# Kernel optimization log

Hardware: AMD Instinct MI355X
Metric: run time of the kernel (lower is better)

The kernel has to match this reference:

```python
import jax, jax.numpy as jnp
import numpy as np

NEG_SLOPE = 0.2  # PyG GATConv default negative_slope
EPS = 1e-16


def gat_conv(x, edge_index, W, att_src, att_dst, bias, heads, out_c, concat):
    """Faithful PyG GATConv forward (add_self_loops=True).
    x: [N, F_in], edge_index: [2, E] (row 0 = src, row 1 = dst),
    W: [heads*out_c, F_in], att_src/att_dst: [1, heads, out_c], bias: [out]
    """
    N = x.shape[0]
    loop = jnp.arange(N, dtype=edge_index.dtype)
    src = jnp.concatenate([edge_index[0], loop])
    dst = jnp.concatenate([edge_index[1], loop])

    h = (x @ W.T).reshape(N, heads, out_c)            # [N, H, C]
    a_src = jnp.sum(h * att_src, axis=-1)             # [N, H]
    a_dst = jnp.sum(h * att_dst, axis=-1)             # [N, H]

    e = jax.nn.leaky_relu(a_src[src] + a_dst[dst], NEG_SLOPE)   # [E+N, H]
    # numerically-stable segment softmax over incoming edges of dst
    m = jax.ops.segment_max(e, dst, num_segments=N)             # [N, H]
    p = jnp.exp(e - m[dst])
    denom = jax.ops.segment_sum(p, dst, num_segments=N)         # [N, H]
    alpha = p / (denom[dst] + EPS)                              # [E+N, H]

    out = jax.ops.segment_sum(h[src] * alpha[:, :, None], dst, num_segments=N)  # [N, H, C]
    out = out.reshape(N, heads * out_c) if concat else out.mean(axis=1)
    return out + bias


def setup_inputs() -> dict:
    key = jax.random.key(0)
    ks = jax.random.split(key, 11)
    N, E = 100_000, 1_600_000
    in_dim, hid, heads = 128, 64, 2
    s = 0.1
    x = jax.random.normal(ks[0], (N, in_dim), jnp.float32)
    edge_index_l2 = jax.random.randint(ks[1], (2, E), 0, N, dtype=jnp.int32)
    edge_index_l1 = jax.random.randint(ks[2], (2, E), 0, N, dtype=jnp.int32)
    # layer gat_l2: in_dim -> hid per head, heads=2, concat=True
    W2 = jax.random.normal(ks[3], (heads * hid, in_dim), jnp.float32) * s
    att_src2 = jax.random.normal(ks[4], (1, heads, hid), jnp.float32) * s
    att_dst2 = jax.random.normal(ks[5], (1, heads, hid), jnp.float32) * s
    b2 = jnp.zeros((heads * hid,), jnp.float32)
    # layer gat_l1: hid*heads -> hid, 1 head, concat=False
    W1 = jax.random.normal(ks[6], (hid, heads * hid), jnp.float32) * s
    att_src1 = jax.random.normal(ks[7], (1, 1, hid), jnp.float32) * s
    att_dst1 = jax.random.normal(ks[8], (1, 1, hid), jnp.float32) * s
    b1 = jnp.zeros((hid,), jnp.float32)
    return {
        "x": x,
        "edge_index_l1": edge_index_l1,
        "edge_index_l2": edge_index_l2,
        "W2": W2, "att_src2": att_src2, "att_dst2": att_dst2, "b2": b2,
        "W1": W1, "att_src1": att_src1, "att_dst1": att_dst1, "b1": b1,
    }


def reference(x, edge_index_l1, edge_index_l2, W2, att_src2, att_dst2, b2,
              W1, att_src1, att_dst1, b1):
    h = jax.nn.elu(gat_conv(x, edge_index_l2, W2, att_src2, att_dst2, b2,
                            heads=2, out_c=64, concat=True))    # [N, 128]
    h = jax.nn.elu(gat_conv(h, edge_index_l1, W1, att_src1, att_dst1, b1,
                            heads=1, out_c=64, concat=False))   # [N, 64]
    return h
```

## Files before the change

### kernel.cpp

```cpp
#include <hip/hip_runtime.h>
#include <hip/hip_bf16.h>
#include <math.h>

#define LRELU_SLOPE 0.2f
#define EPS 1e-16f
#define BUCK_SHIFT 8
#define BUCK_NODES 256
#define MAXBUCK 512

typedef __hip_bfloat16 bf16;
typedef __attribute__((ext_vector_type(8))) short bf16x8;
typedef __attribute__((ext_vector_type(4))) float f32x4;

__device__ inline float lrelu(float v) { return v > 0.f ? v : LRELU_SLOPE * v; }
__device__ inline float bflo(unsigned u) { return __uint_as_float(u << 16); }
__device__ inline float bfhi(unsigned u) { return __uint_as_float(u & 0xffff0000u); }
__device__ inline short f2bf(float f) {
  bf16 t = __float2bfloat16(f);
  return *reinterpret_cast<short*>(&t);
}

__global__ void convert_w(const float* __restrict__ W2, unsigned short* __restrict__ Wb2,
                          const float* __restrict__ W1, unsigned short* __restrict__ Wb1) {
  int idx = blockIdx.x * blockDim.x + threadIdx.x;
  if (idx < 16384) {
    Wb2[idx] = (unsigned short)f2bf(W2[idx]);
  } else {
    int i = idx - 16384;
    if (i < 8192) Wb1[i] = (unsigned short)f2bf(W1[i]);
  }
}

template <int EPB>
__global__ __launch_bounds__(256) void partition_kernel(const int* __restrict__ ei, int E,
                                                        int* __restrict__ gcur,
                                                        int* __restrict__ part, int cap,
                                                        int nbuck) {
  __shared__ int cnt[MAXBUCK];
  __shared__ int sbase[MAXBUCK];
  const int tid = threadIdx.x;
  for (int t = tid; t < nbuck; t += 256) cnt[t] = 0;
  __syncthreads();
  const int e0 = blockIdx.x * EPB;
  constexpr int KPT = EPB / 256;
  int sv[KPT], dv[KPT];
#pragma unroll
  for (int k = 0; k < KPT; k++) {
    int e = e0 + tid + k * 256;
    if (e < E) {
      sv[k] = ei[e];
      dv[k] = ei[E + e];
      atomicAdd(&cnt[dv[k] >> BUCK_SHIFT], 1);
    } else {
      dv[k] = -1;
    }
  }
  __syncthreads();
  for (int t = tid; t < nbuck; t += 256) {
    int c = cnt[t];
    if (c) sbase[t] = atomicAdd(&gcur[t], c);
    cnt[t] = 0;
  }
  __syncthreads();
#pragma unroll
  for (int k = 0; k < KPT; k++) {
    if (dv[k] >= 0) {
      int b = dv[k] >> BUCK_SHIFT;
      int pos = sbase[b] + atomicAdd(&cnt[b], 1);
      if (pos < cap) part[(size_t)b * cap + pos] = (sv[k] << 8) | (dv[k] & (BUCK_NODES - 1));
    }
  }
}

template <int H>
__global__ __launch_bounds__(256) void csr_build_kernel(
    const int* __restrict__ part, const int* __restrict__ gcur, int cap,
    const float* __restrict__ asrc, const float* __restrict__ adst, int* __restrict__ eidx,
    float* __restrict__ pcsr, int* __restrict__ rowbeg, int* __restrict__ rowend, int N) {
  extern __shared__ char smem[];
  int* s_sd = (int*)smem;
  int* hist = (int*)(s_sd + cap);
  int* histp = hist + 256;
  int* escanp = histp + 256;
  int* cur = escanp + 256;
  float* s_ad = (float*)(cur + 256);

  const int b = blockIdx.x;
  const int tid = threadIdx.x;
  const int nb0 = b << BUCK_SHIFT;
  const int nn = min(BUCK_NODES, N - nb0);
  const int cnt = min(gcur[b], cap - 7 * BUCK_NODES);
  const int B = b * cap;

  hist[tid] = 0;
  cur[tid] = 0;
  for (int t = tid; t < nn * H; t += 256) s_ad[t] = adst[(size_t)nb0 * H + t];
  __syncthreads();
  for (int i = tid; i < cnt; i += 256) {
    int pr = part[(size_t)B + i];
    s_sd[i] = pr;
    atomicAdd(&hist[pr & (BUCK_NODES - 1)], 1);
  }
  __syncthreads();
  int hp = (hist[tid] + 7) & ~7;
  histp[tid] = hp;
  escanp[tid] = hp;
  __syncthreads();
  for (int off = 1; off < 256; off <<= 1) {
    int t = (tid >= off) ? escanp[tid - off] : 0;
    __syncthreads();
    escanp[tid] += t;
    __syncthreads();
  }
  if (tid < nn) {
    rowbeg[nb0 + tid] = B + escanp[tid] - histp[tid];
    rowend[nb0 + tid] = B + escanp[tid];
  }
  __syncthreads();
  for (int i = tid; i < cnt; i += 256) {
    int pr = s_sd[i];
    int d8 = pr & (BUCK_NODES - 1);
    int s = pr >> 8;
    int slot = B + (escanp[d8] - histp[d8]) + atomicAdd(&cur[d8], 1);
    eidx[slot] = s;
    if constexpr (H == 2) {
      float2 a = *(const float2*)&asrc[2 * (size_t)s];
      float2 ad = *(const float2*)&s_ad[2 * d8];
      float2 pv;
      pv.x = __expf(lrelu(a.x + ad.x));
      pv.y = __expf(lrelu(a.y + ad.y));
      *(float2*)&pcsr[2 * (size_t)slot] = pv;
    } else {
      pcsr[slot] = __expf(lrelu(asrc[s] + s_ad[d8]));
    }
  }
  if (tid < nn) {
    int base = B + escanp[tid] - histp[tid];
    for (int k = hist[tid]; k < histp[tid]; k++) {
      eidx[base + k] = nb0 + tid;
      if constexpr (H == 2) {
        *(float2*)&pcsr[2 * (size_t)(base + k)] = make_float2(0.f, 0.f);
      } else {
        pcsr[base + k] = 0.f;
      }
    }
  }
}

template <int M, int H, bool SPLIT, typename Tin>
__global__ __launch_bounds__(256) void gemm_att_mfma(
    const Tin* __restrict__ x, const unsigned short* __restrict__ Wb,
    const float* __restrict__ atts, const float* __restrict__ attd, bf16* __restrict__ h,
    float* __restrict__ asrc, float* __restrict__ adst, int N) {
  constexpr int K = 128;
  constexpr int NF = M / 16;
  const int wid = threadIdx.x >> 6;
  const int lane = threadIdx.x & 63;
  const int r0 = blockIdx.x * 64 + wid * 16;
  if (r0 >= N) return;
  const int colb = lane & 15;
  const int kgrp = lane >> 4;
  const size_t arow = (size_t)min(r0 + colb, N - 1);

  f32x4 acc[NF];
#pragma unroll
  for (int f = 0; f < NF; f++) acc[f] = (f32x4){0.f, 0.f, 0.f, 0.f};

#pragma unroll
  for (int k0 = 0; k0 < K; k0 += 32) {
    const int kb = k0 + kgrp * 8;
    bf16x8 ahi, alo;
    if constexpr (SPLIT) {
      const float* xp = (const float*)x + arow * K + kb;
      float4 l0 = *(const float4*)xp;
      float4 l1 = *(const float4*)(xp + 4);
      float xv[8] = {l0.x, l0.y, l0.z, l0.w, l1.x, l1.y, l1.z, l1.w};
#pragma unroll
      for (int j = 0; j < 8; j++) {
        short hb = f2bf(xv[j]);
        ahi[j] = hb;
        float hf = __uint_as_float(((unsigned)(unsigned short)hb) << 16);
        alo[j] = f2bf(xv[j] - hf);
      }
    } else {
      ahi = *(const bf16x8*)((const unsigned short*)x + arow * K + kb);
    }
#pragma unroll
    for (int f = 0; f < NF; f++) {
      bf16x8 b = *(const bf16x8*)(Wb + (size_t)(f * 16 + colb) * K + kb);
      if constexpr (SPLIT)
        acc[f] = __builtin_amdgcn_mfma_f32_16x16x32_bf16(alo, b, acc[f], 0, 0, 0);
      acc[f] = __builtin_amdgcn_mfma_f32_16x16x32_bf16(ahi, b, acc[f], 0, 0, 0);
    }
  }

#pragma unroll
  for (int r = 0; r < 4; r++) {
    const int row = r0 + kgrp * 4 + r;
    const bool ok = row < N;
    float s0 = 0.f, d0 = 0.f, s1 = 0.f, d1 = 0.f;
#pragma unroll
    for (int f = 0; f < NF; f++) {
      float v = acc[f][r];
      int c = f * 16 + colb;
      if (ok) h[(size_t)row * M + c] = __float2bfloat16(v);
      float av = atts[c], dv = attd[c];
      if (H == 2 && f >= NF / 2) {
        s1 += v * av;
        d1 += v * dv;
      } else {
        s0 += v * av;
        d0 += v * dv;
      }
    }
#pragma unroll
    for (int off = 1; off < 16; off <<= 1) {
      s0 += __shfl_xor(s0, off);
      d0 += __shfl_xor(d0, off);
      if (H == 2) {
        s1 += __shfl_xor(s1, off);
        d1 += __shfl_xor(d1, off);
      }
    }
    if (ok && colb == 0) {
      if (H == 2) {
        asrc[2 * (size_t)row] = s0;
        asrc[2 * (size_t)row + 1] = s1;
        adst[2 * (size_t)row] = d0;
        adst[2 * (size_t)row + 1] = d1;
      } else {
        asrc[row] = s0;
        adst[row] = d0;
      }
    }
  }
}

__global__ void gather2_kernel(const bf16* __restrict__ h, const float* __restrict__ asrc,
                               const float* __restrict__ adst, const int* __restrict__ rowbeg,
                               const int* __restrict__ rowend, const int* __restrict__ eidx,
                               const float* __restrict__ pcsr, const float* __restrict__ bias,
                               bf16* __restrict__ outp, int N) {
  long long gt = (long long)blockIdx.x * blockDim.x + threadIdx.x;
  int n = (int)(gt >> 6);
  int lane = threadIdx.x & 63;
  if (n >= N) return;
  int start = rowbeg[n];
  int end = rowend[n];
  const float2 as = *(const float2*)&asrc[2 * (size_t)n];
  const float2 ad = *(const float2*)&adst[2 * (size_t)n];
  float p0 = __expf(lrelu(as.x + ad.x));
  float p1 = __expf(lrelu(as.y + ad.y));
  float den0 = p0, den1 = p1;
  const bool h0 = lane < 32;
  float p = h0 ? p0 : p1;
  unsigned hv = *(const unsigned*)&h[(size_t)n * 128 + 2 * lane];
  float acc0 = p * bflo(hv), acc1 = p * bfhi(hv);
  for (int j = start; j < end; j += 8) {
    int4 ia = *(const int4*)&eidx[j];
    int4 ib = *(const int4*)&eidx[j + 4];
    float4 q0 = *(const float4*)&pcsr[2 * (size_t)j];
    float4 q1 = *(const float4*)&pcsr[2 * (size_t)j + 4];
    float4 q2 = *(const float4*)&pcsr[2 * (size_t)j + 8];
    float4 q3 = *(const float4*)&pcsr[2 * (size_t)j + 12];
    unsigned hA = *(const unsigned*)&h[(size_t)ia.x * 128 + 2 * lane];
    unsigned hB = *(const unsigned*)&h[(size_t)ia.y * 128 + 2 * lane];
    unsigned hC = *(const unsigned*)&h[(size_t)ia.z * 128 + 2 * lane];
    unsigned hD = *(const unsigned*)&h[(size_t)ia.w * 128 + 2 * lane];
    unsigned hE = *(const unsigned*)&h[(size_t)ib.x * 128 + 2 * lane];
    unsigned hF = *(const unsigned*)&h[(size_t)ib.y * 128 + 2 * lane];
    unsigned hG = *(const unsigned*)&h[(size_t)ib.z * 128 + 2 * lane];
    unsigned hH = *(const unsigned*)&h[(size_t)ib.w * 128 + 2 * lane];
    den0 += (q0.x + q0.z) + (q1.x + q1.z) + (q2.x + q2.z) + (q3.x + q3.z);
    den1 += (q0.y + q0.w) + (q1.y + q1.w) + (q2.y + q2.w) + (q3.y + q3.w);
    float pa = h0 ? q0.x : q0.y;
    float pb = h0 ? q0.z : q0.w;
    float pc = h0 ? q1.x : q1.y;
    float pd = h0 ? q1.z : q1.w;
    float pe = h0 ? q2.x : q2.y;
    float pf = h0 ? q2.z : q2.w;
    float pg = h0 ? q3.x : q3.y;
    float ph = h0 ? q3.z : q3.w;
    acc0 += (pa * bflo(hA) + pb * bflo(hB)) + (pc * bflo(hC) + pd * bflo(hD)) +
            (pe * bflo(hE) + pf * bflo(hF)) + (pg * bflo(hG) + ph * bflo(hH));
    acc1 += (pa * bfhi(hA) + pb * bfhi(hB)) + (pc * bfhi(hC) + pd * bfhi(hD)) +
            (pe * bfhi(hE) + pf * bfhi(hF)) + (pg * bfhi(hG) + ph * bfhi(hH));
  }
  float den = (h0 ? den0 : den1) + EPS;
  int c = 2 * lane;
  float v0 = acc0 / den + bias[c];
  float v1 = acc1 / den + bias[c + 1];
  v0 = v0 > 0.f ? v0 : expm1f(v0);
  v1 = v1 > 0.f ? v1 : expm1f(v1);
  __hip_bfloat162 o;
  o.x = __float2bfloat16(v0);
  o.y = __float2bfloat16(v1);
  *(__hip_bfloat162*)&outp[(size_t)n * 128 + c] = o;
}

__global__ void gather1_kernel(const bf16* __restrict__ h, const float* __restrict__ asrc,
                               const float* __restrict__ adst, const int* __restrict__ rowbeg,
                               const int* __restrict__ rowend, const int* __restrict__ eidx,
                               const float* __restrict__ pcsr, const float* __restrict__ bias,
                               float* __restrict__ outp, int N) {
  long long gt = (long long)blockIdx.x * blockDim.x + threadIdx.x;
  int n = (int)(gt >> 6);
  int lane = threadIdx.x & 63;
  if (n >= N) return;
  const int half = lane >> 5;
  const int c = lane & 31;
  int start = rowbeg[n];
  int end = rowend[n];
  float pself = __expf(lrelu(asrc[n] + adst[n]));
  unsigned hv = *(const unsigned*)&h[(size_t)n * 64 + 2 * c];
  float g = half ? 0.f : pself;
  float den = g;
  float acc0 = g * bflo(hv), acc1 = g * bfhi(hv);
  for (int t = start + half * 4; t < end; t += 8) {
    int4 ia = *(const int4*)&eidx[t];
    float4 pa = *(const float4*)&pcsr[t];
    unsigned hA = *(const unsigned*)&h[(size_t)ia.x * 64 + 2 * c];
    unsigned hB = *(const unsigned*)&h[(size_t)ia.y * 64 + 2 * c];
    unsigned hC = *(const unsigned*)&h[(size_t)ia.z * 64 + 2 * c];
    unsigned hD = *(const unsigned*)&h[(size_t)ia.w * 64 + 2 * c];
    den += (pa.x + pa.y) + (pa.z + pa.w);
    acc0 += (pa.x * bflo(hA) + pa.y * bflo(hB)) + (pa.z * bflo(hC) + pa.w * bflo(hD));
    acc1 += (pa.x * bfhi(hA) + pa.y * bfhi(hB)) + (pa.z * bfhi(hC) + pa.w * bfhi(hD));
  }
  den += __shfl_xor(den, 32);
  acc0 += __shfl_xor(acc0, 32);
  acc1 += __shfl_xor(acc1, 32);
  float vden = den + EPS;
  float2 bv = *(const float2*)&bias[2 * c];
  float v0 = acc0 / vden + bv.x;
  float v1 = acc1 / vden + bv.y;
  v0 = v0 > 0.f ? v0 : expm1f(v0);
  v1 = v1 > 0.f ? v1 : expm1f(v1);
  if (!half) *(float2*)&outp[(size_t)n * 64 + 2 * c] = make_float2(v0, v1);
}

extern "C" void kernel_launch(void* const* d_in, const int* in_sizes, int n_in,
                              void* d_out, int out_size, void* d_ws, size_t ws_size,
                              hipStream_t stream) {
  const float* x = (const float*)d_in[0];
  const int* ei1 = (const int*)d_in[1];
  const int* ei2 = (const int*)d_in[2];
  const float* W2 = (const float*)d_in[3];
  const float* as2 = (const float*)d_in[4];
  const float* ad2 = (const float*)d_in[5];
  const float* b2 = (const float*)d_in[6];
  const float* W1 = (const float*)d_in[7];
  const float* as1 = (const float*)d_in[8];
  const float* ad1 = (const float*)d_in[9];
  const float* b1 = (const float*)d_in[10];
  float* out = (float*)d_out;

  const int N = in_sizes[0] / 128;
  const int E1 = in_sizes[1] / 2;
  const int E2 = in_sizes[2] / 2;
  const int Emax = E1 > E2 ? E1 : E2;
  const size_t Ns = (size_t)N;

  const int nbuck = (N + BUCK_NODES - 1) / BUCK_NODES;
  int lam = (Emax + nbuck - 1) / nbuck;
  int cap = lam + (lam >> 2) + 2048;
  cap = (cap + 255) & ~(int)255;
  const size_t NC = (size_t)nbuck * cap;

  float* ws = (float*)d_ws;
  size_t o = 0;
  unsigned short* Wb2 = (unsigned short*)(ws + o); o += 8192;
  unsigned short* Wb1 = (unsigned short*)(ws + o); o += 4096;
  float* asrc2 = ws + o;  o += 2 * Ns;
  float* adst2 = ws + o;  o += 2 * Ns;
  float* asrc1 = ws + o;  o += Ns;
  float* adst1 = ws + o;  o += Ns;
  int* gcur2 = (int*)(ws + o);   o += (size_t)nbuck;
  int* gcur1 = (int*)(ws + o);   o += (size_t)nbuck;
  int* rowbeg2 = (int*)(ws + o); o += Ns;
  int* rowend2 = (int*)(ws + o); o += Ns;
  int* rowbeg1 = (int*)(ws + o); o += Ns;
  int* rowend1 = (int*)(ws + o); o += Ns;
  o = (o + 7) & ~(size_t)7;
  int* part = (int*)(ws + o);    o += NC;
  int* eidx = (int*)(ws + o);    o += NC;
  o = (o + 7) & ~(size_t)7;
  float* pcsr = ws + o;          o += 2 * NC;
  o = (o + 7) & ~(size_t)7;
  bf16* h2 = (bf16*)(ws + o);    o += 64 * Ns;
  bf16* h1 = h2;
  bf16* hin1 = (bf16*)(ws + o);  o += 64 * Ns;

  const size_t smem2 = (size_t)cap * 4 + 4 * 256 * 4 + 2 * 256 * 4 + 64;
  const size_t smem1 = (size_t)cap * 4 + 4 * 256 * 4 + 1 * 256 * 4 + 64;

  convert_w<<<(16384 + 8192 + 255) / 256, 256, 0, stream>>>(W2, Wb2, W1, Wb1);
  hipMemsetAsync(gcur2, 0, 2 * (size_t)nbuck * sizeof(int), stream);

  partition_kernel<4096><<<(E2 + 4095) / 4096, 256, 0, stream>>>(ei2, E2, gcur2, part, cap, nbuck);
  gemm_att_mfma<128, 2, true, float>
      <<<(N + 63) / 64, 256, 0, stream>>>(x, Wb2, as2, ad2, h2, asrc2, adst2, N);
  csr_build_kernel<2><<<nbuck, 256, smem2, stream>>>(part, gcur2, cap, asrc2, adst2, eidx, pcsr,
                                                     rowbeg2, rowend2, N);
  partition_kernel<4096><<<(E1 + 4095) / 4096, 256, 0, stream>>>(ei1, E1, gcur1, part, cap, nbuck);
  gather2_kernel<<<(N + 3) / 4, 256, 0, stream>>>(h2, asrc2, adst2, rowbeg2, rowend2, eidx, pcsr,
                                                  b2, hin1, N);

  gemm_att_mfma<64, 1, false, bf16>
      <<<(N + 63) / 64, 256, 0, stream>>>(hin1, Wb1, as1, ad1, h1, asrc1, adst1, N);
  csr_build_kernel<1><<<nbuck, 256, smem1, stream>>>(part, gcur1, cap, asrc1, adst1, eidx, pcsr,
                                                     rowbeg1, rowend1, N);
  gather1_kernel<<<(N + 3) / 4, 256, 0, stream>>>(h1, asrc1, adst1, rowbeg1, rowend1, eidx, pcsr,
                                                  b1, out, N);
}
```

Before: 324.4 us.

## Split edge weights into per-head planes and half-wave edge split in gather2

Edge attention weights for the two-head layer are now stored as two separate planes instead of interleaved pairs. The layer-2 gather splits each wave into two halves that take alternating groups of four edges, and each lane handles four channels through 8-byte loads. Partial sums are combined with a cross-half shuffle before the output is written. The workspace memset is also folded into the weight-conversion kernel to save one launch, and the per-channel division becomes a multiply by a reciprocal.

```diff
diff --git a/kernel.cpp b/kernel.cpp
--- a/kernel.cpp
+++ b/kernel.cpp
@@ -19,10 +19,15 @@
   bf16 t = __float2bfloat16(f);
   return *reinterpret_cast<short*>(&t);
 }
-
-__global__ void convert_w(const float* __restrict__ W2, unsigned short* __restrict__ Wb2,
-                          const float* __restrict__ W1, unsigned short* __restrict__ Wb1) {
+__device__ inline unsigned pack2(float lo, float hi) {
+  return ((unsigned)(unsigned short)f2bf(hi) << 16) | (unsigned)(unsigned short)f2bf(lo);
+}
+
+__global__ void prep_kernel(const float* __restrict__ W2, unsigned short* __restrict__ Wb2,
+                            const float* __restrict__ W1, unsigned short* __restrict__ Wb1,
+                            int* __restrict__ gcur, int ngc) {
   int idx = blockIdx.x * blockDim.x + threadIdx.x;
+  if (idx < ngc) gcur[idx] = 0;
   if (idx < 16384) {
     Wb2[idx] = (unsigned short)f2bf(W2[idx]);
   } else {
@@ -76,7 +81,8 @@
 __global__ __launch_bounds__(256) void csr_build_kernel(
     const int* __restrict__ part, const int* __restrict__ gcur, int cap,
     const float* __restrict__ asrc, const float* __restrict__ adst, int* __restrict__ eidx,
-    float* __restrict__ pcsr, int* __restrict__ rowbeg, int* __restrict__ rowend, int N) {
+    float* __restrict__ pcsr, int plane, int* __restrict__ rowbeg, int* __restrict__ rowend,
+    int N) {
   extern __shared__ char smem[];
   int* s_sd = (int*)smem;
   int* hist = (int*)(s_sd + cap);
@@ -126,10 +132,8 @@
     if constexpr (H == 2) {
       float2 a = *(const float2*)&asrc[2 * (size_t)s];
       float2 ad = *(const float2*)&s_ad[2 * d8];
-      float2 pv;
-      pv.x = __expf(lrelu(a.x + ad.x));
-      pv.y = __expf(lrelu(a.y + ad.y));
-      *(float2*)&pcsr[2 * (size_t)slot] = pv;
+      pcsr[slot] = __expf(lrelu(a.x + ad.x));
+      pcsr[plane + slot] = __expf(lrelu(a.y + ad.y));
     } else {
       pcsr[slot] = __expf(lrelu(asrc[s] + s_ad[d8]));
     }
@@ -138,11 +142,8 @@
     int base = B + escanp[tid] - histp[tid];
     for (int k = hist[tid]; k < histp[tid]; k++) {
       eidx[base + k] = nb0 + tid;
-      if constexpr (H == 2) {
-        *(float2*)&pcsr[2 * (size_t)(base + k)] = make_float2(0.f, 0.f);
-      } else {
-        pcsr[base + k] = 0.f;
-      }
+      pcsr[base + k] = 0.f;
+      if constexpr (H == 2) pcsr[plane + base + k] = 0.f;
     }
   }
 }
@@ -239,63 +240,60 @@
 __global__ void gather2_kernel(const bf16* __restrict__ h, const float* __restrict__ asrc,
                                const float* __restrict__ adst, const int* __restrict__ rowbeg,
                                const int* __restrict__ rowend, const int* __restrict__ eidx,
-                               const float* __restrict__ pcsr, const float* __restrict__ bias,
-                               bf16* __restrict__ outp, int N) {
+                               const float* __restrict__ pcsr, int plane,
+                               const float* __restrict__ bias, bf16* __restrict__ outp, int N) {
   long long gt = (long long)blockIdx.x * blockDim.x + threadIdx.x;
   int n = (int)(gt >> 6);
   int lane = threadIdx.x & 63;
   if (n >= N) return;
+  const int half = lane >> 5;
+  const int cc = lane & 31;
+  const float* pc = pcsr + ((cc < 16) ? 0 : plane);
   int start = rowbeg[n];
   int end = rowend[n];
   const float2 as = *(const float2*)&asrc[2 * (size_t)n];
   const float2 ad = *(const float2*)&adst[2 * (size_t)n];
   float p0 = __expf(lrelu(as.x + ad.x));
   float p1 = __expf(lrelu(as.y + ad.y));
-  float den0 = p0, den1 = p1;
-  const bool h0 = lane < 32;
-  float p = h0 ? p0 : p1;
-  unsigned hv = *(const unsigned*)&h[(size_t)n * 128 + 2 * lane];
-  float acc0 = p * bflo(hv), acc1 = p * bfhi(hv);
-  for (int j = start; j < end; j += 8) {
+  float g = half ? 0.f : (cc < 16 ? p0 : p1);
+  uint2 hv = *(const uint2*)&h[(size_t)n * 128 + 4 * cc];
+  float den = g;
+  float a0 = g * bflo(hv.x), a1 = g * bfhi(hv.x);
+  float a2 = g * bflo(hv.y), a3 = g * bfhi(hv.y);
+  for (int j = start + half * 4; j < end; j += 8) {
     int4 ia = *(const int4*)&eidx[j];
-    int4 ib = *(const int4*)&eidx[j + 4];
-    float4 q0 = *(const float4*)&pcsr[2 * (size_t)j];
-    float4 q1 = *(const float4*)&pcsr[2 * (size_t)j + 4];
-    float4 q2 = *(const float4*)&pcsr[2 * (size_t)j + 8];
-    float4 q3 = *(const float4*)&pcsr[2 * (size_t)j + 12];
-    unsigned hA = *(const unsigned*)&h[(size_t)ia.x * 128 + 2 * lane];
-    unsigned hB = *(const unsigned*)&h[(size_t)ia.y * 128 + 2 * lane];
-    unsigned hC = *(const unsigned*)&h[(size_t)ia.z * 128 + 2 * lane];
-    unsigned hD = *(const unsigned*)&h[(size_t)ia.w * 128 + 2 * lane];
-    unsigned hE = *(const unsigned*)&h[(size_t)ib.x * 128 + 2 * lane];
-    unsigned hF = *(const unsigned*)&h[(size_t)ib.y * 128 + 2 * lane];
-    unsigned hG = *(const unsigned*)&h[(size_t)ib.z * 128 + 2 * lane];
-    unsigned hH = *(const unsigned*)&h[(size_t)ib.w * 128 + 2 * lane];
-    den0 += (q0.x + q0.z) + (q1.x + q1.z) + (q2.x + q2.z) + (q3.x + q3.z);
-    den1 += (q0.y + q0.w) + (q1.y + q1.w) + (q2.y + q2.w) + (q3.y + q3.w);
-    float pa = h0 ? q0.x : q0.y;
-    float pb = h0 ? q0.z : q0.w;
-    float pc = h0 ? q1.x : q1.y;
-    float pd = h0 ? q1.z : q1.w;
-    float pe = h0 ? q2.x : q2.y;
-    float pf = h0 ? q2.z : q2.w;
-    float pg = h0 ? q3.x : q3.y;
-    float ph = h0 ? q3.z : q3.w;
-    acc0 += (pa * bflo(hA) + pb * bflo(hB)) + (pc * bflo(hC) + pd * bflo(hD)) +
-            (pe * bflo(hE) + pf * bflo(hF)) + (pg * bflo(hG) + ph * bflo(hH));
-    acc1 += (pa * bfhi(hA) + pb * bfhi(hB)) + (pc * bfhi(hC) + pd * bfhi(hD)) +
-            (pe * bfhi(hE) + pf * bfhi(hF)) + (pg * bfhi(hG) + ph * bfhi(hH));
-  }
-  float den = (h0 ? den0 : den1) + EPS;
-  int c = 2 * lane;
-  float v0 = acc0 / den + bias[c];
-  float v1 = acc1 / den + bias[c + 1];
-  v0 = v0 > 0.f ? v0 : expm1f(v0);
-  v1 = v1 > 0.f ? v1 : expm1f(v1);
-  __hip_bfloat162 o;
-  o.x = __float2bfloat16(v0);
-  o.y = __float2bfloat16(v1);
-  *(__hip_bfloat162*)&outp[(size_t)n * 128 + c] = o;
+    float4 pv = *(const float4*)&pc[j];
+    uint2 hA = *(const uint2*)&h[(size_t)ia.x * 128 + 4 * cc];
+    uint2 hB = *(const uint2*)&h[(size_t)ia.y * 128 + 4 * cc];
+    uint2 hC = *(const uint2*)&h[(size_t)ia.z * 128 + 4 * cc];
+    uint2 hD = *(const uint2*)&h[(size_t)ia.w * 128 + 4 * cc];
+    den += (pv.x + pv.y) + (pv.z + pv.w);
+    a0 += (pv.x * bflo(hA.x) + pv.y * bflo(hB.x)) + (pv.z * bflo(hC.x) + pv.w * bflo(hD.x));
+    a1 += (pv.x * bfhi(hA.x) + pv.y * bfhi(hB.x)) + (pv.z * bfhi(hC.x) + pv.w * bfhi(hD.x));
+    a2 += (pv.x * bflo(hA.y) + pv.y * bflo(hB.y)) + (pv.z * bflo(hC.y) + pv.w * bflo(hD.y));
+    a3 += (pv.x * bfhi(hA.y) + pv.y * bfhi(hB.y)) + (pv.z * bfhi(hC.y) + pv.w * bfhi(hD.y));
+  }
+  den += __shfl_xor(den, 32);
+  a0 += __shfl_xor(a0, 32);
+  a1 += __shfl_xor(a1, 32);
+  a2 += __shfl_xor(a2, 32);
+  a3 += __shfl_xor(a3, 32);
+  if (!half) {
+    float rden = 1.f / (den + EPS);
+    float4 bv = *(const float4*)&bias[4 * cc];
+    float v0 = a0 * rden + bv.x;
+    float v1 = a1 * rden + bv.y;
+    float v2 = a2 * rden + bv.z;
+    float v3 = a3 * rden + bv.w;
+    v0 = v0 > 0.f ? v0 : expm1f(v0);
+    v1 = v1 > 0.f ? v1 : expm1f(v1);
+    v2 = v2 > 0.f ? v2 : expm1f(v2);
+    v3 = v3 > 0.f ? v3 : expm1f(v3);
+    uint2 o;
+    o.x = pack2(v0, v1);
+    o.y = pack2(v2, v3);
+    *(uint2*)&outp[(size_t)n * 128 + 4 * cc] = o;
+  }
 }
 
 __global__ void gather1_kernel(const bf16* __restrict__ h, const float* __restrict__ asrc,
@@ -330,13 +328,15 @@
   den += __shfl_xor(den, 32);
   acc0 += __shfl_xor(acc0, 32);
   acc1 += __shfl_xor(acc1, 32);
-  float vden = den + EPS;
-  float2 bv = *(const float2*)&bias[2 * c];
-  float v0 = acc0 / vden + bv.x;
-  float v1 = acc1 / vden + bv.y;
-  v0 = v0 > 0.f ? v0 : expm1f(v0);
-  v1 = v1 > 0.f ? v1 : expm1f(v1);
-  if (!half) *(float2*)&outp[(size_t)n * 64 + 2 * c] = make_float2(v0, v1);
+  if (!half) {
+    float rden = 1.f / (den + EPS);
+    float2 bv = *(const float2*)&bias[2 * c];
+    float v0 = acc0 * rden + bv.x;
+    float v1 = acc1 * rden + bv.y;
+    v0 = v0 > 0.f ? v0 : expm1f(v0);
+    v1 = v1 > 0.f ? v1 : expm1f(v1);
+    *(float2*)&outp[(size_t)n * 64 + 2 * c] = make_float2(v0, v1);
+  }
 }
 
 extern "C" void kernel_launch(void* const* d_in, const int* in_sizes, int n_in,
@@ -394,22 +394,21 @@
   const size_t smem2 = (size_t)cap * 4 + 4 * 256 * 4 + 2 * 256 * 4 + 64;
   const size_t smem1 = (size_t)cap * 4 + 4 * 256 * 4 + 1 * 256 * 4 + 64;
 
-  convert_w<<<(16384 + 8192 + 255) / 256, 256, 0, stream>>>(W2, Wb2, W1, Wb1);
-  hipMemsetAsync(gcur2, 0, 2 * (size_t)nbuck * sizeof(int), stream);
+  prep_kernel<<<(16384 + 8192 + 255) / 256, 256, 0, stream>>>(W2, Wb2, W1, Wb1, gcur2, 2 * nbuck);
 
   partition_kernel<4096><<<(E2 + 4095) / 4096, 256, 0, stream>>>(ei2, E2, gcur2, part, cap, nbuck);
   gemm_att_mfma<128, 2, true, float>
       <<<(N + 63) / 64, 256, 0, stream>>>(x, Wb2, as2, ad2, h2, asrc2, adst2, N);
   csr_build_kernel<2><<<nbuck, 256, smem2, stream>>>(part, gcur2, cap, asrc2, adst2, eidx, pcsr,
-                                                     rowbeg2, rowend2, N);
+                                                     (int)NC, rowbeg2, rowend2, N);
   partition_kernel<4096><<<(E1 + 4095) / 4096, 256, 0, stream>>>(ei1, E1, gcur1, part, cap, nbuck);
   gather2_kernel<<<(N + 3) / 4, 256, 0, stream>>>(h2, asrc2, adst2, rowbeg2, rowend2, eidx, pcsr,
-                                                  b2, hin1, N);
+                                                  (int)NC, b2, hin1, N);
 
   gemm_att_mfma<64, 1, false, bf16>
       <<<(N + 63) / 64, 256, 0, stream>>>(hin1, Wb1, as1, ad1, h1, asrc1, adst1, N);
   csr_build_kernel<1><<<nbuck, 256, smem1, stream>>>(part, gcur1, cap, asrc1, adst1, eidx, pcsr,
-                                                     rowbeg1, rowend1, N);
+                                                     0, rowbeg1, rowend1, N);
   gather1_kernel<<<(N + 3) / 4, 256, 0, stream>>>(h1, asrc1, adst1, rowbeg1, rowend1, eidx, pcsr,
                                                   b1, out, N);
 }
```

Measured after the change: 337.4 us. +4.0%, slower.
